# Kernel optimization log

Hardware: AMD Instinct MI355X
Metric: run time of the kernel (lower is better)

## Reference

```python
import jax, jax.numpy as jnp
import numpy as np

N = 100000   # nodes
E = 1600000  # edges (avg degree 16)
H = 8        # heads
C = 64       # per-head channels
G = 64       # graphs in batch
IN = 3       # input channels
OUT = 10     # classes
NEG_SLOPE = 0.2  # PyG GATConv default


def setup_inputs() -> dict:
    key = jax.random.key(0)
    ks = jax.random.split(key, 16)
    s = 0.1
    return {
        "x": jax.random.normal(ks[0], (N, IN), jnp.float32),
        "edge_index": jax.random.randint(ks[1], (2, E), 0, N),
        "batch": jnp.sort(jax.random.randint(ks[2], (N,), 0, G)),
        "W1": jax.random.normal(ks[3], (IN, H * C), jnp.float32) * s,
        "a1s": jax.random.normal(ks[4], (H, C), jnp.float32) * s,
        "a1d": jax.random.normal(ks[5], (H, C), jnp.float32) * s,
        "b1": jnp.zeros((H * C,), jnp.float32),
        "W2": jax.random.normal(ks[6], (H * C, H * C), jnp.float32) * s,
        "a2s": jax.random.normal(ks[7], (H, C), jnp.float32) * s,
        "a2d": jax.random.normal(ks[8], (H, C), jnp.float32) * s,
        "b2": jnp.zeros((H * C,), jnp.float32),
        "Wc": jax.random.normal(ks[9], (H * C, OUT), jnp.float32) * s,
        "bc": jnp.zeros((OUT,), jnp.float32),
    }


def _gat_layer(x, W, a_s, a_d, b, src, dst, n):
    # h: [N, H, C] per-head projected features
    h = (x @ W).reshape(n, H, C)
    # per-node attention logits per head
    al_s = jnp.einsum('nhc,hc->nh', h, a_s)
    al_d = jnp.einsum('nhc,hc->nh', h, a_d)
    # per-edge raw scores, [E', H]
    e = jax.nn.leaky_relu(al_s[src] + al_d[dst], NEG_SLOPE)
    # segment softmax over incoming edges of each destination node
    m = jax.ops.segment_max(e, dst, num_segments=n)
    ex = jnp.exp(e - m[dst])
    den = jax.ops.segment_sum(ex, dst, num_segments=n)
    alpha = ex / den[dst]  # [E', H]
    # weighted scatter-aggregate of source messages
    out = jax.ops.segment_sum(alpha[:, :, None] * h[src], dst, num_segments=n)
    return out.reshape(n, H * C) + b


def reference(x, edge_index, batch, W1, a1s, a1d, b1, W2, a2s, a2d, b2, Wc, bc):
    n = x.shape[0]
    ar = jnp.arange(n)
    # PyG GATConv adds self-loops by default
    src = jnp.concatenate([edge_index[0], ar])
    dst = jnp.concatenate([edge_index[1], ar])

    x1 = jax.nn.elu(_gat_layer(x, W1, a1s, a1d, b1, src, dst, n))
    x2 = jax.nn.elu(_gat_layer(x1, W2, a2s, a2d, b2, src, dst, n))

    # global mean pool over graphs
    sums = jax.ops.segment_sum(x2, batch, num_segments=G)
    cnt = jax.ops.segment_sum(jnp.ones((n, 1), x2.dtype), batch, num_segments=G)
    pooled = sums / jnp.maximum(cnt, 1.0)
    return pooled @ Wc + bc
```

## Files before the change

kernel.cpp:

```cpp
#include <hip/hip_runtime.h>
#include <math.h>

#define N_NODES 100000
#define N_EDGES 1600000
#define EP (N_EDGES + N_NODES)
#define NH 8
#define NC 64
#define NG 64
#define HC 512
#define BCAP 64
#define NPART 32
#define BPSTR 80

typedef unsigned short bf16_t;
typedef unsigned char fp8_t;
typedef __attribute__((ext_vector_type(8))) short short8;
typedef __attribute__((ext_vector_type(4))) float floatx4;
typedef __attribute__((ext_vector_type(2))) float floatx2;

__device__ inline float bf2f(bf16_t u) {
    union { unsigned int i; float f; } x;
    x.i = (unsigned int)u << 16;
    return x.f;
}
__device__ inline bf16_t f2bf(float f) {
    union { float f; unsigned int i; } x;
    x.f = f;
    unsigned int b = x.i;
    return (bf16_t)((b + 0x7fffu + ((b >> 16) & 1u)) >> 16);
}
__device__ inline fp8_t f2fp8(float f) {
    int v = __builtin_amdgcn_cvt_pk_fp8_f32(f, f, 0, false);
    return (fp8_t)v;
}

__device__ inline void ldsload16(const void* g, void* l) {
    __builtin_amdgcn_global_load_lds(
        (const __attribute__((address_space(1))) unsigned int*)g,
        (__attribute__((address_space(3))) unsigned int*)l, 16, 0, 0);
}

#define NBW2T (HC * HC / 256)
#define FB_PACK ((N_NODES + 255) / 256)
#define FB_SCAT ((EP + 255) / 256)
__global__ void k_setup(const float* __restrict__ x, bf16_t* __restrict__ xb,
                        const int* __restrict__ batch, int* __restrict__ gstart,
                        const int* __restrict__ ei, int* __restrict__ cnt,
                        int* __restrict__ csr,
                        const float* __restrict__ W1, const float* __restrict__ a1s,
                        const float* __restrict__ a1d, float* __restrict__ wprep,
                        const float* __restrict__ W2, bf16_t* __restrict__ W2T) {
    int blk = blockIdx.x;
    if (blk < FB_PACK) {
        int i = blk * 256 + threadIdx.x;
        if (i < N_NODES) {
            ushort4 p;
            p.x = f2bf(x[i * 3 + 0]);
            p.y = f2bf(x[i * 3 + 1]);
            p.z = f2bf(x[i * 3 + 2]);
            p.w = 0;
            *(ushort4*)&xb[i * 4] = p;
            int b = batch[i];
            if (i == 0) {
                for (int g = 0; g <= b; g++) gstart[g] = 0;
            } else {
                int bp = batch[i - 1];
                if (b != bp)
                    for (int g = bp + 1; g <= b; g++) gstart[g] = i;
            }
            if (i == N_NODES - 1)
                for (int g = b + 1; g <= NG; g++) gstart[g] = N_NODES;
        }
        return;
    }
    blk -= FB_PACK;
    if (blk < FB_SCAT) {
        int i = blk * 256 + threadIdx.x;
        if (i >= EP) return;
        int s, d;
        if (i < N_EDGES) { s = ei[i]; d = ei[N_EDGES + i]; }
        else { s = i - N_EDGES; d = s; }
        int pos = atomicAdd(&cnt[d], 1);
        csr[d * BCAP + pos] = s;
        return;
    }
    blk -= FB_SCAT;
    if (blk < NBW2T) {
        int i = blk * 256 + threadIdx.x;
        int n = i >> 9, kp = i & 511;
        int k = (kp & 7) * 64 + (kp >> 3);
        W2T[i] = f2bf(W2[k * HC + n]);
        return;
    }
    int t = threadIdx.x;
    if (t < 48) {
        int isD = t >= 24;
        int tt = t % 24;
        int h = tt / 3, k = tt % 3;
        const float* a = isD ? a1d : a1s;
        float s = 0.f;
        for (int c = 0; c < 64; c++) s += W1[k * HC + h * 64 + c] * a[h * 64 + c];
        wprep[t] = s;
    }
}

__global__ __launch_bounds__(64) void k_layer1(
    const bf16_t* __restrict__ xb, const int* __restrict__ cnt, const int* __restrict__ csr,
    const float* __restrict__ W1, const float* __restrict__ wprep, const float* __restrict__ b1,
    bf16_t* __restrict__ x1p) {
    __shared__ float wp[48];
    int lane = threadIdx.x;
    if (lane < 48) wp[lane] = wprep[lane];
    __syncthreads();
    int half = lane >> 5, l32 = lane & 31;
    int dst = blockIdx.x * 2 + half;
    int rs = dst * BCAP, re = rs + cnt[dst];
    ushort4 xd4 = *(const ushort4*)&xb[dst * 4];
    float xdx = bf2f(xd4.x), xdy = bf2f(xd4.y), xdz = bf2f(xd4.z);
    float ald[NH];
#pragma unroll
    for (int h = 0; h < NH; h++)
        ald[h] = xdx * wp[24 + h * 3] + xdy * wp[24 + h * 3 + 1] + xdz * wp[24 + h * 3 + 2];
    float den[NH], c0[NH], c1[NH], c2[NH];
#pragma unroll
    for (int h = 0; h < NH; h++) { den[h] = 0.f; c0[h] = 0.f; c1[h] = 0.f; c2[h] = 0.f; }
    for (int base = rs; base < re; base += 32) {
        int e = base + l32;
        if (e < re) {
            int s = csr[e];
            ushort4 sv4 = *(const ushort4*)&xb[s * 4];
            float svx = bf2f(sv4.x), svy = bf2f(sv4.y), svz = bf2f(sv4.z);
#pragma unroll
            for (int h = 0; h < NH; h++) {
                float ev = svx * wp[h * 3] + svy * wp[h * 3 + 1] + svz * wp[h * 3 + 2] + ald[h];
                ev = fmaxf(ev, 0.2f * ev);
                float w = __expf(ev);
                den[h] += w;
                c0[h] += w * svx;
                c1[h] += w * svy;
                c2[h] += w * svz;
            }
        }
    }
#pragma unroll
    for (int h = 0; h < NH; h++) {
#pragma unroll
        for (int off = 1; off < 32; off <<= 1) {
            den[h] += __shfl_xor(den[h], off, 64);
            c0[h] += __shfl_xor(c0[h], off, 64);
            c1[h] += __shfl_xor(c1[h], off, 64);
            c2[h] += __shfl_xor(c2[h], off, 64);
        }
    }
    bf16_t vbA[NH], vbB[NH];
#pragma unroll
    for (int h = 0; h < NH; h++) {
        int colA = h * 64 + l32;
        float vA = c0[h] * W1[colA] + c1[h] * W1[HC + colA] + c2[h] * W1[2 * HC + colA];
        vA = vA / den[h] + b1[colA];
        vA = vA > 0.f ? vA : (__expf(vA) - 1.f);
        vbA[h] = f2bf(vA);
        int colB = colA + 32;
        float vB = c0[h] * W1[colB] + c1[h] * W1[HC + colB] + c2[h] * W1[2 * HC + colB];
        vB = vB / den[h] + b1[colB];
        vB = vB > 0.f ? vB : (__expf(vB) - 1.f);
        vbB[h] = f2bf(vB);
    }
    uint4 oA, oB;
    oA.x = (unsigned int)vbA[0] | ((unsigned int)vbA[1] << 16);
    oA.y = (unsigned int)vbA[2] | ((unsigned int)vbA[3] << 16);
    oA.z = (unsigned int)vbA[4] | ((unsigned int)vbA[5] << 16);
    oA.w = (unsigned int)vbA[6] | ((unsigned int)vbA[7] << 16);
    oB.x = (unsigned int)vbB[0] | ((unsigned int)vbB[1] << 16);
    oB.y = (unsigned int)vbB[2] | ((unsigned int)vbB[3] << 16);
    oB.z = (unsigned int)vbB[4] | ((unsigned int)vbB[5] << 16);
    oB.w = (unsigned int)vbB[6] | ((unsigned int)vbB[7] << 16);
    *(uint4*)&x1p[(size_t)dst * HC + l32 * 8] = oA;
    *(uint4*)&x1p[(size_t)dst * HC + (l32 + 32) * 8] = oB;
}

__global__ __launch_bounds__(256) void k_gemm2(const bf16_t* __restrict__ A,
                                               const bf16_t* __restrict__ BT,
                                               fp8_t* __restrict__ Out,
                                               int row_base, int nrows,
                                               const float* __restrict__ a2s,
                                               const float* __restrict__ a2d,
                                               float* __restrict__ al2s,
                                               float* __restrict__ al2d) {
    __shared__ short smem[16384];
    short* As = smem;
    short* Bs = smem + 8192;
    int tid = threadIdx.x;
    int lane = tid & 63, wave = tid >> 6;
    int wm = wave & 1, wn = wave >> 1;
    int lm = lane & 15, quad = lane >> 4;
    int gx = blockIdx.x, gy = blockIdx.y;
    int l8 = lane >> 3, lc8 = lane & 7;
    int sw = lc8 ^ l8;
    const bf16_t* ga[4];
    const bf16_t* gb[4];
    short* la[4];
    short* lb[4];
#pragma unroll
    for (int it = 0; it < 4; it++) {
        int ar = gy * 128 + wave * 32 + it * 8 + l8;
        int arc = (ar < nrows) ? ar : 0;
        ga[it] = A + (size_t)(row_base + arc) * HC + sw * 8;
        gb[it] = BT + (size_t)(gx * 128 + wave * 32 + it * 8 + l8) * HC + sw * 8;
        la[it] = As + (wave * 32 + it * 8) * 64;
        lb[it] = Bs + (wave * 32 + it * 8) * 64;
    }

    floatx4 acc[4][4];
#pragma unroll
    for (int mi = 0; mi < 4; mi++)
#pragma unroll
        for (int ni = 0; ni < 4; ni++) acc[mi][ni] = (floatx4){0.f, 0.f, 0.f, 0.f};

    int lmw = lm & 7;
    for (int k0 = 0; k0 < HC; k0 += 64) {
        __syncthreads();
#pragma unroll
        for (int it = 0; it < 4; it++) ldsload16(ga[it] + k0, la[it]);
#pragma unroll
        for (int it = 0; it < 4; it++) ldsload16(gb[it] + k0, lb[it]);
        __syncthreads();
        short8 af[4][2], bf[4][2];
#pragma unroll
        for (int mi = 0; mi < 4; mi++)
#pragma unroll
            for (int kk = 0; kk < 2; kk++) {
                int pos = (kk * 4 + quad) ^ lmw;
                af[mi][kk] = *(const short8*)&As[(wm * 64 + mi * 16 + lm) * 64 + pos * 8];
            }
#pragma unroll
        for (int ni = 0; ni < 4; ni++)
#pragma unroll
            for (int kk = 0; kk < 2; kk++) {
                int pos = (kk * 4 + quad) ^ lmw;
                bf[ni][kk] = *(const short8*)&Bs[(wn * 64 + ni * 16 + lm) * 64 + pos * 8];
            }
#pragma unroll
        for (int mi = 0; mi < 4; mi++)
#pragma unroll
            for (int ni = 0; ni < 4; ni++) {
                acc[mi][ni] = __builtin_amdgcn_mfma_f32_16x16x32_bf16(af[mi][0], bf[ni][0], acc[mi][ni], 0, 0, 0);
                acc[mi][ni] = __builtin_amdgcn_mfma_f32_16x16x32_bf16(af[mi][1], bf[ni][1], acc[mi][ni], 0, 0, 0);
            }
    }
    int head = gx * 2 + wn;
    float a2sv[4], a2dv[4];
#pragma unroll
    for (int ni = 0; ni < 4; ni++) {
        int col = gx * 128 + wn * 64 + ni * 16 + lm;
        a2sv[ni] = a2s[col];
        a2dv[ni] = a2d[col];
    }
#pragma unroll
    for (int mi = 0; mi < 4; mi++) {
#pragma unroll
        for (int rg = 0; rg < 4; rg++) {
            int lrow = gy * 128 + wm * 64 + mi * 16 + quad * 4 + rg;
            float ps = 0.f, pd = 0.f;
#pragma unroll
            for (int ni = 0; ni < 4; ni++) {
                float v = acc[mi][ni][rg];
                ps += v * a2sv[ni];
                pd += v * a2dv[ni];
            }
#pragma unroll
            for (int off = 1; off < 16; off <<= 1) {
                ps += __shfl_xor(ps, off, 64);
                pd += __shfl_xor(pd, off, 64);
            }
            if (lrow < nrows && lm == 0) {
                int ar = row_base + lrow;
                al2s[ar * NH + head] = ps;
                al2d[ar * NH + head] = pd;
            }
        }
    }
    __syncthreads();
    unsigned char* bpatch = (unsigned char*)smem + wave * (32 * BPSTR);
#pragma unroll
    for (int p = 0; p < 2; p++) {
#pragma unroll
        for (int mih = 0; mih < 2; mih++) {
            int mi = p * 2 + mih;
#pragma unroll
            for (int ni = 0; ni < 4; ni++)
#pragma unroll
                for (int rg = 0; rg < 4; rg++) {
                    int rl = mih * 16 + quad * 4 + rg;
                    bpatch[rl * BPSTR + ni * 16 + lm] = f2fp8(acc[mi][ni][rg]);
                }
        }
#pragma unroll
        for (int it = 0; it < 2; it++) {
            int idx = it * 64 + lane;
            int rl = idx >> 2, c16 = idx & 3;
            uint4 v = *(uint4*)&bpatch[rl * BPSTR + c16 * 16];
            int lrow = gy * 128 + wm * 64 + p * 32 + rl;
            if (lrow < nrows)
                *(uint4*)&Out[(size_t)lrow * HC + wn * 64 + gx * 128 + c16 * 16] = v;
        }
    }
}

#define ACC8(v, w) do { floatx2 c_;                                                            \
    c_ = __builtin_amdgcn_cvt_pk_f32_fp8((v).x, false); acc[0] += (w) * c_.x; acc[1] += (w) * c_.y; \
    c_ = __builtin_amdgcn_cvt_pk_f32_fp8((v).x, true);  acc[2] += (w) * c_.x; acc[3] += (w) * c_.y; \
    c_ = __builtin_amdgcn_cvt_pk_f32_fp8((v).y, false); acc[4] += (w) * c_.x; acc[5] += (w) * c_.y; \
    c_ = __builtin_amdgcn_cvt_pk_f32_fp8((v).y, true);  acc[6] += (w) * c_.x; acc[7] += (w) * c_.y; \
} while (0)

__global__ __launch_bounds__(64) void k_layer2pool(
    const fp8_t* __restrict__ h2lo, const fp8_t* __restrict__ h2hi, int srows,
    const float* __restrict__ al2s, const float* __restrict__ al2d,
    const int* __restrict__ cnt, const int* __restrict__ csr, const float* __restrict__ b2,
    const int* __restrict__ batch, float* __restrict__ poolpart) {
    __shared__ float wlds[528];
    __shared__ int slds[64];
    __shared__ __align__(16) fp8_t gbuf[4096];
    int lane = threadIdx.x;
    int hme = lane >> 3;
    int hb = hme * 65;
    int dst = blockIdx.x;
    int rs = dst * BCAP, re = rs + cnt[dst];
    float4 d0 = *(const float4*)&al2d[dst * NH];
    float4 d1 = *(const float4*)&al2d[dst * NH + 4];
    float ald[NH] = {d0.x, d0.y, d0.z, d0.w, d1.x, d1.y, d1.z, d1.w};
    float den[NH], acc[8];
#pragma unroll
    for (int h = 0; h < NH; h++) den[h] = 0.f;
#pragma unroll
    for (int q = 0; q < 8; q++) acc[q] = 0.f;
    int lhalf = lane >> 5;
    int l31 = lane & 31;
    for (int eb = rs; eb < re; eb += 64) {
        int e = eb + lane;
        int cl = re - eb; if (cl > 64) cl = 64;
        float w[NH];
        int s = 0;
        if (e < re) {
            s = csr[e];
            float4 p0 = *(const float4*)&al2s[s * NH];
            float4 p1 = *(const float4*)&al2s[s * NH + 4];
            float als[NH] = {p0.x, p0.y, p0.z, p0.w, p1.x, p1.y, p1.z, p1.w};
#pragma unroll
            for (int h = 0; h < NH; h++) {
                float ev = als[h] + ald[h];
                ev = fmaxf(ev, 0.2f * ev);
                w[h] = __expf(ev);
                den[h] += w[h];
            }
        } else {
#pragma unroll
            for (int h = 0; h < NH; h++) w[h] = 0.f;
        }
        slds[lane] = s;
#pragma unroll
        for (int h = 0; h < NH; h++) wlds[h * 65 + lane] = w[h];
        int nb = cl >> 2;
        if (nb > 0) {
#pragma unroll
            for (int t = 0; t < 2; t++) {
                int s0 = slds[t * 2 + lhalf];
                const fp8_t* bp = (s0 < srows) ? (h2lo + (size_t)s0 * HC)
                                               : (h2hi + (size_t)(s0 - srows) * HC);
                ldsload16(bp + l31 * 16, &gbuf[t * 1024]);
            }
            for (int k = 0; k < nb; k++) {
                if (k + 1 < nb) {
                    int hoff = ((k + 1) & 1) * 2048;
#pragma unroll
                    for (int t = 0; t < 2; t++) {
                        int s0 = slds[(k + 1) * 4 + t * 2 + lhalf];
                        const fp8_t* bp = (s0 < srows) ? (h2lo + (size_t)s0 * HC)
                                                       : (h2hi + (size_t)(s0 - srows) * HC);
                        ldsload16(bp + l31 * 16, &gbuf[hoff + t * 1024]);
                    }
                    asm volatile("s_waitcnt vmcnt(2)" ::: "memory");
                } else {
                    asm volatile("s_waitcnt vmcnt(0)" ::: "memory");
                }
                __builtin_amdgcn_sched_barrier(0);
                int coff = (k & 1) * 2048;
#pragma unroll
                for (int u = 0; u < 4; u++) {
                    float wA = wlds[hb + k * 4 + u];
                    uint2 vA = *(const uint2*)&gbuf[coff + u * 512 + lane * 8];
                    ACC8(vA, wA);
                }
            }
        }
        for (int j = nb * 4; j < cl; j++) {
            int sA = slds[j];
            float wA = wlds[hb + j];
            const fp8_t* bA = (sA < srows) ? (h2lo + (size_t)sA * HC)
                                           : (h2hi + (size_t)(sA - srows) * HC);
            uint2 vA = *(const uint2*)&bA[lane * 8];
            ACC8(vA, wA);
        }
    }
#pragma unroll
    for (int h = 0; h < NH; h++)
#pragma unroll
        for (int off = 1; off < 64; off <<= 1) den[h] += __shfl_xor(den[h], off, 64);
    float dd = den[0];
#pragma unroll
    for (int h = 1; h < NH; h++) dd = (hme == h) ? den[h] : dd;
    float dinv = 1.0f / dd;
    float4 ba = *(const float4*)&b2[lane * 8];
    float4 bb = *(const float4*)&b2[lane * 8 + 4];
    float bv[8] = {ba.x, ba.y, ba.z, ba.w, bb.x, bb.y, bb.z, bb.w};
#pragma unroll
    for (int q = 0; q < 8; q++) {
        float v = acc[q] * dinv + bv[q];
        v = v > 0.f ? v : (__expf(v) - 1.f);
        int c = lane * 8 + q;
        wlds[c + (c >> 5)] = v;
    }
    int g = batch[dst];
    float* pp = poolpart + ((size_t)(dst & (NPART - 1)) * NG + g) * HC;
#pragma unroll
    for (int h = 0; h < NH; h++) {
        int c = h * 64 + lane;
        atomicAdd(&pp[c], wlds[c + (c >> 5)]);
    }
}

__global__ __launch_bounds__(256) void k_poolcls(const float* __restrict__ poolpart,
                                                 const int* __restrict__ gstart,
                                                 const float* __restrict__ Wc,
                                                 const float* __restrict__ bc,
                                                 float* __restrict__ out) {
    __shared__ float pl[512];
    int g = blockIdx.x, t = threadIdx.x;
    for (int c = t; c < HC; c += 256) {
        float s = 0.f;
        for (int p = 0; p < NPART; p++) s += poolpart[(size_t)p * NG * HC + g * HC + c];
        pl[c] = s;
    }
    __syncthreads();
    if (t < 10) {
        float cnt = fmaxf((float)(gstart[g + 1] - gstart[g]), 1.0f);
        float acc = 0.f;
        for (int k = 0; k < HC; k++) acc += pl[k] * Wc[k * 10 + t];
        out[g * 10 + t] = acc / cnt + bc[t];
    }
}

extern "C" void kernel_launch(void* const* d_in, const int* in_sizes, int n_in,
                              void* d_out, int out_size, void* d_ws, size_t ws_size,
                              hipStream_t stream) {
    const float* x   = (const float*)d_in[0];
    const int*   ei  = (const int*)d_in[1];
    const int*   bat = (const int*)d_in[2];
    const float* W1  = (const float*)d_in[3];
    const float* a1s = (const float*)d_in[4];
    const float* a1d = (const float*)d_in[5];
    const float* b1  = (const float*)d_in[6];
    const float* W2  = (const float*)d_in[7];
    const float* a2s = (const float*)d_in[8];
    const float* a2d = (const float*)d_in[9];
    const float* b2  = (const float*)d_in[10];
    const float* Wc  = (const float*)d_in[11];
    const float* bc  = (const float*)d_in[12];
    float* out = (float*)d_out;

    char* ws = (char*)d_ws;
    size_t off = 0;
    auto alloc = [&](size_t bytes) {
        size_t o = off;
        off += (bytes + 255) & ~(size_t)255;
        return o;
    };
    float*  wprep    = (float*)(ws + alloc(48 * 4));
    int*    cnt      = (int*)(ws + alloc((size_t)N_NODES * 4));
    int*    gstart   = (int*)(ws + alloc(65 * 4));
    bf16_t* xb       = (bf16_t*)(ws + alloc((size_t)N_NODES * 4 * 2));
    int*    csr      = (int*)(ws + alloc((size_t)N_NODES * BCAP * 4));
    bf16_t* W2T      = (bf16_t*)(ws + alloc((size_t)HC * HC * 2));
    bf16_t* x1b      = (bf16_t*)(ws + alloc((size_t)N_NODES * HC * 2));
    float*  al2s     = (float*)(ws + alloc((size_t)N_NODES * NH * 4));
    float*  al2d     = (float*)(ws + alloc((size_t)N_NODES * NH * 4));
    float*  poolpart = (float*)(ws + alloc((size_t)NPART * NG * HC * 4));

    size_t rem = (ws_size > off) ? ws_size - off : 0;
    int nslices, srows;
    if (rem >= (size_t)N_NODES * HC)      { nslices = 1;  srows = N_NODES; }
    else if (rem >= (size_t)50000 * HC)   { nslices = 2;  srows = 50000; }
    else if (rem >= (size_t)25000 * HC)   { nslices = 4;  srows = 25000; }
    else if (rem >= (size_t)12500 * HC)   { nslices = 8;  srows = 12500; }
    else                                  { nslices = 16; srows = 6250; }
    fp8_t* T = (fp8_t*)(ws + alloc((size_t)srows * HC));
    fp8_t* h2hi = (fp8_t*)x1b;

    hipMemsetAsync(cnt, 0, (size_t)N_NODES * 4, stream);
    hipMemsetAsync(poolpart, 0, (size_t)NPART * NG * HC * 4, stream);

    k_setup<<<FB_PACK + FB_SCAT + NBW2T + 1, 256, 0, stream>>>(
        x, xb, bat, gstart, ei, cnt, csr, W1, a1s, a1d, wprep, W2, W2T);
    k_layer1<<<N_NODES / 2, 64, 0, stream>>>(xb, cnt, csr, W1, wprep, b1, x1b);
    for (int s = 0; s < nslices; s++) {
        fp8_t* outp = (s == 0) ? T : (h2hi + (size_t)(s - 1) * srows * HC);
        k_gemm2<<<dim3(4, (srows + 127) / 128), 256, 0, stream>>>(
            x1b, W2T, outp, s * srows, srows, a2s, a2d, al2s, al2d);
    }
    k_layer2pool<<<N_NODES, 64, 0, stream>>>(T, h2hi, srows, al2s, al2d,
                                             cnt, csr, b2, bat, poolpart);
    k_poolcls<<<NG, 256, 0, stream>>>(poolpart, gstart, Wc, bc, out);
}
```

Before: 644.9 us.

## Process eight destination nodes per block and pre-reduce pooled sums before atomics

The layer-2 aggregate-and-pool kernel now has each 64-thread block handle 8 consecutive destination nodes. Because batch is sorted, it keeps a running per-graph sum in registers and flushes it with atomics only when the graph id changes or the block ends, instead of issuing 512 atomics per node. The slice sizing for the fp8 GEMM buffer also now uses the largest multiple of 128 rows that fits the workspace, replacing fixed power-of-two fractions. In exchange, the kernel launches 8x fewer blocks, each doing serial work, which could lower occupancy and latency hiding.

```diff
diff --git a/kernel.cpp b/kernel.cpp
--- a/kernel.cpp
+++ b/kernel.cpp
@@ -11,6 +11,7 @@
 #define BCAP 64
 #define NPART 32
 #define BPSTR 80
+#define DCHUNK 8
 
 typedef unsigned short bf16_t;
 typedef unsigned char fp8_t;
@@ -325,104 +326,132 @@
     int lane = threadIdx.x;
     int hme = lane >> 3;
     int hb = hme * 65;
-    int dst = blockIdx.x;
-    int rs = dst * BCAP, re = rs + cnt[dst];
-    float4 d0 = *(const float4*)&al2d[dst * NH];
-    float4 d1 = *(const float4*)&al2d[dst * NH + 4];
-    float ald[NH] = {d0.x, d0.y, d0.z, d0.w, d1.x, d1.y, d1.z, d1.w};
-    float den[NH], acc[8];
-#pragma unroll
-    for (int h = 0; h < NH; h++) den[h] = 0.f;
-#pragma unroll
-    for (int q = 0; q < 8; q++) acc[q] = 0.f;
     int lhalf = lane >> 5;
     int l31 = lane & 31;
-    for (int eb = rs; eb < re; eb += 64) {
-        int e = eb + lane;
-        int cl = re - eb; if (cl > 64) cl = 64;
-        float w[NH];
-        int s = 0;
-        if (e < re) {
-            s = csr[e];
-            float4 p0 = *(const float4*)&al2s[s * NH];
-            float4 p1 = *(const float4*)&al2s[s * NH + 4];
-            float als[NH] = {p0.x, p0.y, p0.z, p0.w, p1.x, p1.y, p1.z, p1.w};
-#pragma unroll
-            for (int h = 0; h < NH; h++) {
-                float ev = als[h] + ald[h];
-                ev = fmaxf(ev, 0.2f * ev);
-                w[h] = __expf(ev);
-                den[h] += w[h];
-            }
-        } else {
-#pragma unroll
-            for (int h = 0; h < NH; h++) w[h] = 0.f;
-        }
-        slds[lane] = s;
-#pragma unroll
-        for (int h = 0; h < NH; h++) wlds[h * 65 + lane] = w[h];
-        int nb = cl >> 2;
-        if (nb > 0) {
-#pragma unroll
-            for (int t = 0; t < 2; t++) {
-                int s0 = slds[t * 2 + lhalf];
-                const fp8_t* bp = (s0 < srows) ? (h2lo + (size_t)s0 * HC)
-                                               : (h2hi + (size_t)(s0 - srows) * HC);
-                ldsload16(bp + l31 * 16, &gbuf[t * 1024]);
-            }
-            for (int k = 0; k < nb; k++) {
-                if (k + 1 < nb) {
-                    int hoff = ((k + 1) & 1) * 2048;
-#pragma unroll
-                    for (int t = 0; t < 2; t++) {
-                        int s0 = slds[(k + 1) * 4 + t * 2 + lhalf];
-                        const fp8_t* bp = (s0 < srows) ? (h2lo + (size_t)s0 * HC)
-                                                       : (h2hi + (size_t)(s0 - srows) * HC);
-                        ldsload16(bp + l31 * 16, &gbuf[hoff + t * 1024]);
-                    }
-                    asm volatile("s_waitcnt vmcnt(2)" ::: "memory");
-                } else {
-                    asm volatile("s_waitcnt vmcnt(0)" ::: "memory");
-                }
-                __builtin_amdgcn_sched_barrier(0);
-                int coff = (k & 1) * 2048;
-#pragma unroll
-                for (int u = 0; u < 4; u++) {
-                    float wA = wlds[hb + k * 4 + u];
-                    uint2 vA = *(const uint2*)&gbuf[coff + u * 512 + lane * 8];
-                    ACC8(vA, wA);
-                }
-            }
-        }
-        for (int j = nb * 4; j < cl; j++) {
-            int sA = slds[j];
-            float wA = wlds[hb + j];
-            const fp8_t* bA = (sA < srows) ? (h2lo + (size_t)sA * HC)
-                                           : (h2hi + (size_t)(sA - srows) * HC);
-            uint2 vA = *(const uint2*)&bA[lane * 8];
-            ACC8(vA, wA);
-        }
-    }
-#pragma unroll
-    for (int h = 0; h < NH; h++)
-#pragma unroll
-        for (int off = 1; off < 64; off <<= 1) den[h] += __shfl_xor(den[h], off, 64);
-    float dd = den[0];
-#pragma unroll
-    for (int h = 1; h < NH; h++) dd = (hme == h) ? den[h] : dd;
-    float dinv = 1.0f / dd;
     float4 ba = *(const float4*)&b2[lane * 8];
     float4 bb = *(const float4*)&b2[lane * 8 + 4];
     float bv[8] = {ba.x, ba.y, ba.z, ba.w, bb.x, bb.y, bb.z, bb.w};
+    float pacc[8];
+#pragma unroll
+    for (int q = 0; q < 8; q++) pacc[q] = 0.f;
+    int dst0 = blockIdx.x * DCHUNK;
+    int curg = batch[dst0];
+    int part = blockIdx.x & (NPART - 1);
+    for (int di = 0; di < DCHUNK; di++) {
+        int dst = dst0 + di;
+        int rs = dst * BCAP, re = rs + cnt[dst];
+        float4 d0 = *(const float4*)&al2d[dst * NH];
+        float4 d1 = *(const float4*)&al2d[dst * NH + 4];
+        float ald[NH] = {d0.x, d0.y, d0.z, d0.w, d1.x, d1.y, d1.z, d1.w};
+        float den[NH], acc[8];
+#pragma unroll
+        for (int h = 0; h < NH; h++) den[h] = 0.f;
+#pragma unroll
+        for (int q = 0; q < 8; q++) acc[q] = 0.f;
+        for (int eb = rs; eb < re; eb += 64) {
+            int e = eb + lane;
+            int cl = re - eb; if (cl > 64) cl = 64;
+            float w[NH];
+            int s = 0;
+            if (e < re) {
+                s = csr[e];
+                float4 p0 = *(const float4*)&al2s[s * NH];
+                float4 p1 = *(const float4*)&al2s[s * NH + 4];
+                float als[NH] = {p0.x, p0.y, p0.z, p0.w, p1.x, p1.y, p1.z, p1.w};
+#pragma unroll
+                for (int h = 0; h < NH; h++) {
+                    float ev = als[h] + ald[h];
+                    ev = fmaxf(ev, 0.2f * ev);
+                    w[h] = __expf(ev);
+                    den[h] += w[h];
+                }
+            } else {
+#pragma unroll
+                for (int h = 0; h < NH; h++) w[h] = 0.f;
+            }
+            slds[lane] = s;
+#pragma unroll
+            for (int h = 0; h < NH; h++) wlds[h * 65 + lane] = w[h];
+            int nb = cl >> 2;
+            if (nb > 0) {
+#pragma unroll
+                for (int t = 0; t < 2; t++) {
+                    int s0 = slds[t * 2 + lhalf];
+                    const fp8_t* bp = (s0 < srows) ? (h2lo + (size_t)s0 * HC)
+                                                   : (h2hi + (size_t)(s0 - srows) * HC);
+                    ldsload16(bp + l31 * 16, &gbuf[t * 1024]);
+                }
+                for (int k = 0; k < nb; k++) {
+                    if (k + 1 < nb) {
+                        int hoff = ((k + 1) & 1) * 2048;
+#pragma unroll
+                        for (int t = 0; t < 2; t++) {
+                            int s0 = slds[(k + 1) * 4 + t * 2 + lhalf];
+                            const fp8_t* bp = (s0 < srows) ? (h2lo + (size_t)s0 * HC)
+                                                           : (h2hi + (size_t)(s0 - srows) * HC);
+                            ldsload16(bp + l31 * 16, &gbuf[hoff + t * 1024]);
+                        }
+                        asm volatile("s_waitcnt vmcnt(2)" ::: "memory");
+                    } else {
+                        asm volatile("s_waitcnt vmcnt(0)" ::: "memory");
+                    }
+                    __builtin_amdgcn_sched_barrier(0);
+                    int coff = (k & 1) * 2048;
+#pragma unroll
+                    for (int u = 0; u < 4; u++) {
+                        float wA = wlds[hb + k * 4 + u];
+                        uint2 vA = *(const uint2*)&gbuf[coff + u * 512 + lane * 8];
+                        ACC8(vA, wA);
+                    }
+                }
+            }
+            for (int j = nb * 4; j < cl; j++) {
+                int sA = slds[j];
+                float wA = wlds[hb + j];
+                const fp8_t* bA = (sA < srows) ? (h2lo + (size_t)sA * HC)
+                                               : (h2hi + (size_t)(sA - srows) * HC);
+                uint2 vA = *(const uint2*)&bA[lane * 8];
+                ACC8(vA, wA);
+            }
+        }
+#pragma unroll
+        for (int h = 0; h < NH; h++)
+#pragma unroll
+            for (int off = 1; off < 64; off <<= 1) den[h] += __shfl_xor(den[h], off, 64);
+        float dd = den[0];
+#pragma unroll
+        for (int h = 1; h < NH; h++) dd = (hme == h) ? den[h] : dd;
+        float dinv = 1.0f / dd;
+        int g = batch[dst];
+        if (g != curg) {
+#pragma unroll
+            for (int q = 0; q < 8; q++) {
+                int c = lane * 8 + q;
+                wlds[c + (c >> 5)] = pacc[q];
+            }
+            float* pp = poolpart + ((size_t)part * NG + curg) * HC;
+#pragma unroll
+            for (int h = 0; h < NH; h++) {
+                int c = h * 64 + lane;
+                atomicAdd(&pp[c], wlds[c + (c >> 5)]);
+            }
+#pragma unroll
+            for (int q = 0; q < 8; q++) pacc[q] = 0.f;
+            curg = g;
+        }
+#pragma unroll
+        for (int q = 0; q < 8; q++) {
+            float v = acc[q] * dinv + bv[q];
+            v = v > 0.f ? v : (__expf(v) - 1.f);
+            pacc[q] += v;
+        }
+    }
 #pragma unroll
     for (int q = 0; q < 8; q++) {
-        float v = acc[q] * dinv + bv[q];
-        v = v > 0.f ? v : (__expf(v) - 1.f);
         int c = lane * 8 + q;
-        wlds[c + (c >> 5)] = v;
-    }
-    int g = batch[dst];
-    float* pp = poolpart + ((size_t)(dst & (NPART - 1)) * NG + g) * HC;
+        wlds[c + (c >> 5)] = pacc[q];
+    }
+    float* pp = poolpart + ((size_t)part * NG + curg) * HC;
 #pragma unroll
     for (int h = 0; h < NH; h++) {
         int c = h * 64 + lane;
@@ -488,12 +517,14 @@
     float*  poolpart = (float*)(ws + alloc((size_t)NPART * NG * HC * 4));
 
     size_t rem = (ws_size > off) ? ws_size - off : 0;
-    int nslices, srows;
-    if (rem >= (size_t)N_NODES * HC)      { nslices = 1;  srows = N_NODES; }
-    else if (rem >= (size_t)50000 * HC)   { nslices = 2;  srows = 50000; }
-    else if (rem >= (size_t)25000 * HC)   { nslices = 4;  srows = 25000; }
-    else if (rem >= (size_t)12500 * HC)   { nslices = 8;  srows = 12500; }
-    else                                  { nslices = 16; srows = 6250; }
+    size_t rowcap = rem / HC;
+    int srows;
+    if (rowcap >= (size_t)N_NODES) srows = N_NODES;
+    else {
+        srows = (int)(rowcap & ~(size_t)127);
+        if (srows < 6250) srows = 6250;
+    }
+    int nslices = (N_NODES + srows - 1) / srows;
     fp8_t* T = (fp8_t*)(ws + alloc((size_t)srows * HC));
     fp8_t* h2hi = (fp8_t*)x1b;
 
@@ -505,10 +536,12 @@
     k_layer1<<<N_NODES / 2, 64, 0, stream>>>(xb, cnt, csr, W1, wprep, b1, x1b);
     for (int s = 0; s < nslices; s++) {
         fp8_t* outp = (s == 0) ? T : (h2hi + (size_t)(s - 1) * srows * HC);
-        k_gemm2<<<dim3(4, (srows + 127) / 128), 256, 0, stream>>>(
-            x1b, W2T, outp, s * srows, srows, a2s, a2d, al2s, al2d);
-    }
-    k_layer2pool<<<N_NODES, 64, 0, stream>>>(T, h2hi, srows, al2s, al2d,
-                                             cnt, csr, b2, bat, poolpart);
+        int nrows = N_NODES - s * srows;
+        if (nrows > srows) nrows = srows;
+        k_gemm2<<<dim3(4, (nrows + 127) / 128), 256, 0, stream>>>(
+            x1b, W2T, outp, s * srows, nrows, a2s, a2d, al2s, al2d);
+    }
+    k_layer2pool<<<N_NODES / DCHUNK, 64, 0, stream>>>(T, h2hi, srows, al2s, al2d,
+                                                      cnt, csr, b2, bat, poolpart);
     k_poolcls<<<NG, 256, 0, stream>>>(poolpart, gstart, Wc, bc, out);
 }
```

Result: faster. 587.6 us (-8.9%).
